# Performance work log

Hardware: AMD Instinct MI355X
Metric: run time of the kernel (lower is better)

Reference implementation:

```python
import jax, jax.numpy as jnp
import numpy as np

EPS = 1e-5

def _fm(x):
    # feature_map: exact (erf) GELU + 1, matching torch F.gelu default
    return jax.nn.gelu(x, approximate=False) + 1.0

def _gds(q, k):
    # global_dot_score: reduce over seq dim, broadcast back over seq
    e = (q * k).sum(axis=1)            # [B, D]
    return e[:, None, :] * q           # [B, S, D]

def _attn(q, k, v, scale):
    qf = _fm(q)
    kf = _fm(k)
    e = _gds(qf, kf) / scale           # [B, S, D]
    return jax.nn.softmax(e, axis=1) * v

def _ln(x, g, b):
    mu = x.mean(axis=-1, keepdims=True)
    var = ((x - mu) ** 2).mean(axis=-1, keepdims=True)
    return (x - mu) / jnp.sqrt(var + EPS) * g + b

def setup_inputs() -> dict:
    B, S, D, V, L, O = 8, 2048, 1024, 32000, 2, 2
    key = jax.random.key(0)
    ks = jax.random.split(key, 4)
    src = jax.random.randint(ks[0], (B, S), 0, V, dtype=jnp.int64 if jax.config.jax_enable_x64 else jnp.int32)
    trg = jax.random.randint(ks[1], (B, S), 0, V, dtype=src.dtype)
    emb = jax.random.normal(ks[2], (V, D), dtype=jnp.float32) * 0.02
    Wc = jax.random.normal(ks[3], (D, O), dtype=jnp.float32) * 0.02
    return {
        'src': src, 'trg': trg, 'emb': emb,
        'enc_g': jnp.ones((L, D), jnp.float32), 'enc_b': jnp.zeros((L, D), jnp.float32),
        'dec_ng': jnp.ones((L, D), jnp.float32), 'dec_nb': jnp.zeros((L, D), jnp.float32),
        'dec_tg': jnp.ones((L, D), jnp.float32), 'dec_tb': jnp.zeros((L, D), jnp.float32),
        'Wc': Wc, 'bc': jnp.zeros((O,), jnp.float32),
    }

def reference(src, trg, emb, enc_g, enc_b, dec_ng, dec_nb, dec_tg, dec_tb, Wc, bc):
    D = emb.shape[1]
    L = enc_g.shape[0]
    scale = jnp.sqrt(jnp.asarray(D, emb.dtype))

    # ---------- Encoder ----------
    x = emb[src]                          # [B, S, D]
    ctx = jnp.cumsum(x, axis=1)
    out = _gds(x, ctx)                    # encoder: out becomes rep
    rep = out
    for i in range(L):
        a = _attn(out, ctx, rep, scale)
        out = _ln(a + out, enc_g[i], enc_b[i])
        if i < L - 1:
            ctx = jnp.cumsum(out, axis=1)
            rep = _gds(out, ctx)
    enc_out = out
    enc_ctx = ctx[:, -1:, :]              # [B, 1, D]

    # ---------- Decoder ----------
    xe = emb[trg]
    ctx = jnp.cumsum(xe, axis=1)
    x = _gds(xe, ctx)                     # decoder: x becomes rep
    rep = x
    k2 = enc_ctx                          # [B, 1, D]
    v2 = enc_out.sum(axis=1, keepdims=True)  # [B, 1, D]
    for i in range(L):
        a1 = _attn(x, ctx, rep, scale)
        q = _ln(a1 + x, dec_ng[i], dec_nb[i])
        a2 = _attn(q, k2, v2, scale)      # cross attention (broadcast over seq)
        x = _ln(a2 + q, dec_tg[i], dec_tb[i])
        if i < L - 1:
            ctx = jnp.cumsum(x, axis=1)
            rep = _gds(x, ctx)

    # ---------- Predictor (use='seq', pool='mean') ----------
    pooled = x.mean(axis=1)               # [B, D]
    return pooled @ Wc + bc               # [B, out]
```

## Files before the change

kernel.cpp:

```cpp
#include <hip/hip_runtime.h>
#include <math.h>

namespace {

constexpr int Bb = 8;
constexpr int Ss = 2048;
constexpr int Dd = 1024;
constexpr int D4 = Dd / 4;
constexpr int NC = 256;
constexpr int Sc2 = Ss / NC;
constexpr int Tb = 256;
constexpr int SEG = 8;
constexpr int CPS = NC / SEG;
constexpr float INV_SCALE = 0.03125f;
constexpr float BIG = 3.0e38f;

__device__ __forceinline__ float fast_erf(float z) {
  float az = fabsf(z);
  float t = __builtin_amdgcn_rcpf(fmaf(0.3275911f, az, 1.0f));
  float p = fmaf(1.061405429f, t, -1.453152027f);
  p = fmaf(p, t, 1.421413741f);
  p = fmaf(p, t, -0.284496736f);
  p = fmaf(p, t, 0.254829592f);
  p *= t;
  float e = __expf(-az * az);
  float r = fmaf(-p, e, 1.0f);
  return copysignf(r, z);
}
__device__ __forceinline__ float fm_act(float x) {
  return fmaf(0.5f * x, 1.0f + fast_erf(x * 0.70710678118654752f), 1.0f);
}

__device__ __forceinline__ float4 f4(float v) { return make_float4(v, v, v, v); }
__device__ __forceinline__ float4 add4(float4 a, float4 b) {
  return make_float4(a.x + b.x, a.y + b.y, a.z + b.z, a.w + b.w);
}
__device__ __forceinline__ float4 mul4(float4 a, float4 b) {
  return make_float4(a.x * b.x, a.y * b.y, a.z * b.z, a.w * b.w);
}
__device__ __forceinline__ float4 fma4(float4 a, float4 b, float4 c) {
  return make_float4(fmaf(a.x, b.x, c.x), fmaf(a.y, b.y, c.y), fmaf(a.z, b.z, c.z), fmaf(a.w, b.w, c.w));
}
__device__ __forceinline__ float4 min4(float4 a, float4 b) {
  return make_float4(fminf(a.x, b.x), fminf(a.y, b.y), fminf(a.z, b.z), fminf(a.w, b.w));
}
__device__ __forceinline__ float4 max4(float4 a, float4 b) {
  return make_float4(fmaxf(a.x, b.x), fmaxf(a.y, b.y), fmaxf(a.z, b.z), fmaxf(a.w, b.w));
}
__device__ __forceinline__ float4 fm4(float4 x) {
  return make_float4(fm_act(x.x), fm_act(x.y), fm_act(x.z), fm_act(x.w));
}
__device__ __forceinline__ float4 ld4(const float* p, size_t j4) {
  return reinterpret_cast<const float4*>(p)[j4];
}
__device__ __forceinline__ void st4(float* p, size_t j4, float4 v) {
  reinterpret_cast<float4*>(p)[j4] = v;
}
__device__ __forceinline__ float4 pexp4(float4 ei, float4 qf, float4 M) {
  return make_float4(__expf(fmaf(ei.x, qf.x, -M.x)), __expf(fmaf(ei.y, qf.y, -M.y)),
                     __expf(fmaf(ei.z, qf.z, -M.z)), __expf(fmaf(ei.w, qf.w, -M.w)));
}

__device__ __forceinline__ float blockSum(float v) {
  __shared__ float wsm[Tb / 64];
  for (int off = 32; off > 0; off >>= 1) v += __shfl_down(v, off, 64);
  const int lane = threadIdx.x & 63;
  const int w = threadIdx.x >> 6;
  __syncthreads();
  if (lane == 0) wsm[w] = v;
  __syncthreads();
  return wsm[0] + wsm[1] + wsm[2] + wsm[3];
}

struct GA { const int* tok; float* X; float* cs; float* el; };
struct SA { const float* cs; const float* el; float* off; float* e; float* last; };
struct PA { const float* X; const float* qs; const float* off; float* pe; float* pmn; float* pmx; };
struct MA { const float* pe; const float* pmn; const float* pmx; const float* k2; float* ei; float* Mv; };
struct QA { const float* X; const float* qs; const float* ei; const float* Mv; float* ps; };
struct RA { const float* pp; float* outv; int recip; };
struct LA { float* X; const float* qs; const float* vs; const float* rs; const float* ml;
            const float* ei; const float* Mv; const float* rdv; const float* g; const float* bt;
            float* cs; float* el; float* xe; float* xn; float* xx; };


__global__ __launch_bounds__(Tb) void k_gather(GA a0, GA a1, const float* __restrict__ emb) {
  const GA a = (blockIdx.z == 0) ? a0 : a1;
  const int t = threadIdx.x, c = blockIdx.x, b = blockIdx.y;
  const int* tp = a.tok + b * Ss + c * Sc2;
  float4* xp = reinterpret_cast<float4*>(a.X) + ((size_t)(b * Ss + c * Sc2)) * D4 + t;
  const float4* ep = reinterpret_cast<const float4*>(emb);
  float4 run = f4(0.f), e = f4(0.f);
#pragma unroll
  for (int i = 0; i < Sc2; ++i) {
    float4 v = ep[(size_t)tp[i] * D4 + t];
    xp[(size_t)i * D4] = v;
    run = add4(run, v);
    e = fma4(v, run, e);
  }
  const size_t idx = ((size_t)b * NC + c) * D4 + t;
  st4(a.cs, idx, run);
  st4(a.el, idx, e);
}

__global__ __launch_bounds__(Tb) void k_p1(PA a0, PA a1) {
  const PA a = (blockIdx.z == 0) ? a0 : a1;
  const int t = threadIdx.x, c = blockIdx.x, b = blockIdx.y;
  const size_t idx = ((size_t)b * NC + c) * D4 + t;
  float4 run = ld4(a.off, idx);
  const float4 q4 = a.qs ? ld4(a.qs, (size_t)b * D4 + t) : f4(1.f);
  const float4* xp = reinterpret_cast<const float4*>(a.X) + ((size_t)(b * Ss + c * Sc2)) * D4 + t;
  float4 e = f4(0.f), mn = f4(BIG), mx = f4(0.f);
#pragma unroll
  for (int i = 0; i < Sc2; ++i) {
    float4 x = xp[(size_t)i * D4];
    run = add4(run, x);
    float4 qf = fm4(mul4(q4, x));
    float4 kf = fm4(run);
    e = fma4(qf, kf, e);
    mn = min4(mn, qf);
    mx = max4(mx, qf);
  }
  st4(a.pe, idx, e);
  st4(a.pmn, idx, mn);
  st4(a.pmx, idx, mx);
}

__global__ __launch_bounds__(Tb) void k_p2(QA a0, QA a1) {
  const QA a = (blockIdx.z == 0) ? a0 : a1;
  const int t = threadIdx.x, c = blockIdx.x, b = blockIdx.y;
  const size_t j4 = (size_t)b * D4 + t;
  const float4 q4 = a.qs ? ld4(a.qs, j4) : f4(1.f);
  const float4 e4 = ld4(a.ei, j4);
  const float4 M4 = ld4(a.Mv, j4);
  const float4* xp = reinterpret_cast<const float4*>(a.X) + ((size_t)(b * Ss + c * Sc2)) * D4 + t;
  float4 s = f4(0.f);
#pragma unroll
  for (int i = 0; i < Sc2; ++i) {
    float4 x = xp[(size_t)i * D4];
    float4 qf = fm4(mul4(q4, x));
    s = add4(s, pexp4(e4, qf, M4));
  }
  st4(a.ps, ((size_t)b * NC + c) * D4 + t, s);
}

__global__ __launch_bounds__(Tb) void k_ln(LA a0, LA a1) {
  const LA a = (blockIdx.z == 0) ? a0 : a1;
  __shared__ float red[Sc2][Tb];
  __shared__ float mu_s[Sc2], inv_s[Sc2];
  const int t = threadIdx.x, c = blockIdx.x, b = blockIdx.y;
  float4* xp = reinterpret_cast<float4*>(a.X) + ((size_t)(b * Ss + c * Sc2)) * D4 + t;
  const size_t j4 = (size_t)b * D4 + t;
  const float4 e4 = ld4(a.ei, j4), M4 = ld4(a.Mv, j4), rv4 = ld4(a.rdv, j4);
  const float4 q4 = a.qs ? ld4(a.qs, j4) : f4(1.f);
  const float4 vs4 = a.vs ? ld4(a.vs, j4) : f4(1.f);
  const float4 ml4 = a.ml ? ld4(a.ml, j4) : f4(1.f);
  const float4 rs4 = a.rs ? ld4(a.rs, j4) : f4(1.f);
  float4 vals[Sc2];
#pragma unroll
  for (int i = 0; i < Sc2; ++i) {
    float4 x = xp[(size_t)i * D4];
    float4 qf = fm4(mul4(q4, x));
    float4 p = mul4(pexp4(e4, qf, M4), rv4);
    float4 v = a.ml ? mul4(p, ml4) : mul4(p, mul4(vs4, x));
    float4 val = add4(v, mul4(rs4, x));
    vals[i] = val;
    red[i][t] = val.x + val.y + val.z + val.w;
  }
  __syncthreads();
  const int lane = t & 63, w = t >> 6;
#pragma unroll
  for (int rr = 0; rr < Sc2 / 4; ++rr) {
    const int row = w * (Sc2 / 4) + rr;
    float s = red[row][lane] + red[row][lane + 64] + red[row][lane + 128] + red[row][lane + 192];
    for (int off = 32; off > 0; off >>= 1) s += __shfl_down(s, off, 64);
    if (lane == 0) mu_s[row] = s * (1.0f / Dd);
  }
  __syncthreads();
#pragma unroll
  for (int i = 0; i < Sc2; ++i) {
    const float m = mu_s[i];
    float4 vv = vals[i];
    float aa = vv.x - m, b2 = vv.y - m, c2 = vv.z - m, d2 = vv.w - m;
    red[i][t] = aa * aa + b2 * b2 + c2 * c2 + d2 * d2;
  }
  __syncthreads();
#pragma unroll
  for (int rr = 0; rr < Sc2 / 4; ++rr) {
    const int row = w * (Sc2 / 4) + rr;
    float s = red[row][lane] + red[row][lane + 64] + red[row][lane + 128] + red[row][lane + 192];
    for (int off = 32; off > 0; off >>= 1) s += __shfl_down(s, off, 64);
    if (lane == 0) inv_s[row] = rsqrtf(s * (1.0f / Dd) + 1e-5f);
  }
  __syncthreads();
  const float4 g4 = ld4(a.g, t), b4 = ld4(a.bt, t);
  float4 run = f4(0.f), e = f4(0.f);
  float4 xs = f4(0.f), xmn = f4(BIG), xmx = f4(0.f);
#pragma unroll
  for (int i = 0; i < Sc2; ++i) {
    const float m = mu_s[i], inv = inv_s[i];
    float4 vv = vals[i];
    float4 y;
    y.x = fmaf((vv.x - m) * inv, g4.x, b4.x);
    y.y = fmaf((vv.y - m) * inv, g4.y, b4.y);
    y.z = fmaf((vv.z - m) * inv, g4.z, b4.z);
    y.w = fmaf((vv.w - m) * inv, g4.w, b4.w);
    xp[(size_t)i * D4] = y;
    if (a.cs) {
      run = add4(run, y);
      if (a.el) e = fma4(y, run, e);
    }
    if (a.xe) {
      float4 qfy = fm4(y);
      xs = add4(xs, qfy);
      xmn = min4(xmn, qfy);
      xmx = max4(xmx, qfy);
    }
  }
  const size_t idx = ((size_t)b * NC + c) * D4 + t;
  if (a.cs) st4(a.cs, idx, run);
  if (a.el) st4(a.el, idx, e);
  if (a.xe) {
    st4(a.xe, idx, xs);
    st4(a.xn, idx, xmn);
    st4(a.xx, idx, xmx);
  }
}


__global__ __launch_bounds__(Tb) void t_scan8(SA a0, SA a1) {
  const SA a = (blockIdx.z == 0) ? a0 : a1;
  __shared__ float lds[SEG][32];
  const int tid = threadIdx.x;
  const int jl = tid & 31, seg = tid >> 5;
  const int j = blockIdx.x * 32 + jl;
  const int b = j >> 10, d = j & 1023;
  const size_t base = (size_t)b * NC * Dd + d;
  float s = 0.f;
#pragma unroll 8
  for (int i = 0; i < CPS; ++i) s += a.cs[base + (size_t)(seg * CPS + i) * Dd];
  lds[seg][jl] = s;
  __syncthreads();
  float o = 0.f;
#pragma unroll
  for (int g2 = 0; g2 < SEG; ++g2) { float v = lds[g2][jl]; o += (g2 < seg) ? v : 0.f; }
  __syncthreads();
  float run = o, e = 0.f;
#pragma unroll 8
  for (int i = 0; i < CPS; ++i) {
    const size_t k = base + (size_t)(seg * CPS + i) * Dd;
    float cv = a.cs[k];
    a.off[k] = run;
    e += a.el[k] + run * cv;
    run += cv;
  }
  lds[seg][jl] = e;
  __syncthreads();
  if (seg == 0) {
    float et = 0.f;
#pragma unroll
    for (int g2 = 0; g2 < SEG; ++g2) et += lds[g2][jl];
    a.e[j] = et;
  }
  if (a.last && seg == SEG - 1) a.last[j] = run;
}

__global__ __launch_bounds__(Tb) void t_m8(MA a0, MA a1) {
  const MA a = (blockIdx.z == 0) ? a0 : a1;
  __shared__ float le[SEG][32], lmn[SEG][32], lmx[SEG][32];
  const int tid = threadIdx.x;
  const int jl = tid & 31, seg = tid >> 5;
  const int j = blockIdx.x * 32 + jl;
  const int b = j >> 10, d = j & 1023;
  const size_t base = (size_t)b * NC * Dd + d;
  float ec = 0.f, mn = BIG, mx = 0.f;
#pragma unroll 8
  for (int i = 0; i < CPS; ++i) {
    const size_t k = base + (size_t)(seg * CPS + i) * Dd;
    ec += a.pe[k];
    mn = fminf(mn, a.pmn[k]);
    mx = fmaxf(mx, a.pmx[k]);
  }
  le[seg][jl] = ec; lmn[seg][jl] = mn; lmx[seg][jl] = mx;
  __syncthreads();
  if (seg == 0) {
#pragma unroll
    for (int g2 = 1; g2 < SEG; ++g2) {
      ec += le[g2][jl];
      mn = fminf(mn, lmn[g2][jl]);
      mx = fmaxf(mx, lmx[g2][jl]);
    }
    if (a.k2) ec *= fm_act(a.k2[j]);
    const float e2 = ec * INV_SCALE;
    a.ei[j] = e2;
    a.Mv[j] = (ec >= 0.f) ? e2 * mx : e2 * mn;
  }
}

__global__ __launch_bounds__(Tb) void t_red8(RA a0, RA a1) {
  const RA a = (blockIdx.z == 0) ? a0 : a1;
  __shared__ float lds[SEG][32];
  const int tid = threadIdx.x;
  const int jl = tid & 31, seg = tid >> 5;
  const int j = blockIdx.x * 32 + jl;
  const int b = j >> 10, d = j & 1023;
  const size_t base = (size_t)b * NC * Dd + d;
  float s = 0.f;
#pragma unroll 8
  for (int i = 0; i < CPS; ++i) s += a.pp[base + (size_t)(seg * CPS + i) * Dd];
  lds[seg][jl] = s;
  __syncthreads();
  if (seg == 0) {
#pragma unroll
    for (int g2 = 1; g2 < SEG; ++g2) s += lds[g2][jl];
    a.outv[j] = a.recip ? 1.0f / s : s;
  }
}

__global__ __launch_bounds__(Tb) void k_final(const float* __restrict__ pooled, const float* __restrict__ Wc,
    const float* __restrict__ bc, float* __restrict__ out) {
  const int b = blockIdx.x, t = threadIdx.x;
  float4 acc = ld4(pooled, (size_t)b * D4 + t);
  float4 w0 = ld4(Wc, 2 * t), w1 = ld4(Wc, 2 * t + 1);
  float s0 = acc.x * w0.x + acc.y * w0.z + acc.z * w1.x + acc.w * w1.z;
  float s1 = acc.x * w0.y + acc.y * w0.w + acc.z * w1.y + acc.w * w1.w;
  s0 = blockSum(s0);
  s1 = blockSum(s1);
  if (t == 0) {
    out[b * 2 + 0] = s0 * (1.0f / Ss) + bc[0];
    out[b * 2 + 1] = s1 * (1.0f / Ss) + bc[1];
  }
}

}

extern "C" void kernel_launch(void* const* d_in, const int* in_sizes, int n_in,
                              void* d_out, int out_size, void* d_ws, size_t ws_size,
                              hipStream_t stream) {
  (void)in_sizes; (void)n_in; (void)out_size; (void)ws_size;
  const int* src = (const int*)d_in[0];
  const int* trg = (const int*)d_in[1];
  const float* emb = (const float*)d_in[2];
  const float* enc_g = (const float*)d_in[3];
  const float* enc_b = (const float*)d_in[4];
  const float* dec_ng = (const float*)d_in[5];
  const float* dec_nb = (const float*)d_in[6];
  const float* dec_tg = (const float*)d_in[7];
  const float* dec_tb = (const float*)d_in[8];
  const float* Wc = (const float*)d_in[9];
  const float* bc = (const float*)d_in[10];
  float* out = (float*)d_out;

  float* ws = (float*)d_ws;
  const size_t TEN = (size_t)Bb * Ss * Dd;
  const size_t MM = (size_t)Bb * NC * Dd;
  float* A0 = ws;
  float* A1 = A0 + TEN;
  float* p = A1 + TEN;
  float* csE = p; p += MM;  float* elE = p; p += MM;  float* offE = p; p += MM;
  float* peE = p; p += MM;  float* pmnE = p; p += MM; float* pmxE = p; p += MM;
  float* psE = p; p += MM;
  float* csD = p; p += MM;  float* elD = p; p += MM;  float* offD = p; p += MM;
  float* peD = p; p += MM;  float* pmnD = p; p += MM; float* pmxD = p; p += MM;
  float* psD = p; p += MM;
  const int BD = Bb * Dd;
  float* e0E = p; p += BD;  float* e1E = p; p += BD;
  float* e0D = p; p += BD;  float* e1D = p; p += BD;
  float* eiE = p; p += BD;  float* MvE = p; p += BD;  float* rdvE = p; p += BD;
  float* eiD = p; p += BD;  float* MvD = p; p += BD;  float* rdvD = p; p += BD;
  float* ectx = p; p += BD; float* v2 = p; p += BD;   float* pooled = p; p += BD;

  const dim3 g2(NC, Bb, 2), g1(NC, Bb, 1);
  const dim3 t2(BD / 32, 1, 2), t1(BD / 32, 1, 1);

  k_gather<<<g2, Tb, 0, stream>>>(GA{src, A0, csE, elE}, GA{trg, A1, csD, elD}, emb);
  t_scan8<<<t2, Tb, 0, stream>>>(SA{csE, elE, offE, e0E, nullptr}, SA{csD, elD, offD, e0D, nullptr});
  k_p1<<<g2, Tb, 0, stream>>>(PA{A0, e0E, offE, peE, pmnE, pmxE}, PA{A1, e0D, offD, peD, pmnD, pmxD});
  t_m8<<<t2, Tb, 0, stream>>>(MA{peE, pmnE, pmxE, nullptr, eiE, MvE}, MA{peD, pmnD, pmxD, nullptr, eiD, MvD});
  k_p2<<<g2, Tb, 0, stream>>>(QA{A0, e0E, eiE, MvE, psE}, QA{A1, e0D, eiD, MvD, psD});
  t_red8<<<t2, Tb, 0, stream>>>(RA{psE, rdvE, 1}, RA{psD, rdvD, 1});
  k_ln<<<g2, Tb, 0, stream>>>(
      LA{A0, e0E, e0E, e0E, nullptr, eiE, MvE, rdvE, enc_g, enc_b, csE, elE, nullptr, nullptr, nullptr},
      LA{A1, e0D, e0D, e0D, nullptr, eiD, MvD, rdvD, dec_ng, dec_nb, nullptr, nullptr, peD, pmnD, pmxD});

  t_scan8<<<t1, Tb, 0, stream>>>(SA{csE, elE, offE, e1E, ectx}, SA{csE, elE, offE, e1E, ectx});
  k_p1<<<g1, Tb, 0, stream>>>(PA{A0, nullptr, offE, peE, pmnE, pmxE}, PA{A0, nullptr, offE, peE, pmnE, pmxE});
  t_m8<<<t1, Tb, 0, stream>>>(MA{peE, pmnE, pmxE, nullptr, eiE, MvE}, MA{peE, pmnE, pmxE, nullptr, eiE, MvE});
  k_p2<<<g1, Tb, 0, stream>>>(QA{A0, nullptr, eiE, MvE, psE}, QA{A0, nullptr, eiE, MvE, psE});
  t_red8<<<t1, Tb, 0, stream>>>(RA{psE, rdvE, 1}, RA{psE, rdvE, 1});
  k_ln<<<g1, Tb, 0, stream>>>(
      LA{A0, nullptr, e1E, nullptr, nullptr, eiE, MvE, rdvE, enc_g + Dd, enc_b + Dd, csE, nullptr, nullptr, nullptr, nullptr},
      LA{A0, nullptr, e1E, nullptr, nullptr, eiE, MvE, rdvE, enc_g + Dd, enc_b + Dd, csE, nullptr, nullptr, nullptr, nullptr});
  t_red8<<<t1, Tb, 0, stream>>>(RA{csE, v2, 0}, RA{csE, v2, 0});

  t_m8<<<t1, Tb, 0, stream>>>(MA{peD, pmnD, pmxD, ectx, eiD, MvD}, MA{peD, pmnD, pmxD, ectx, eiD, MvD});
  k_p2<<<g1, Tb, 0, stream>>>(QA{A1, nullptr, eiD, MvD, psD}, QA{A1, nullptr, eiD, MvD, psD});
  t_red8<<<t1, Tb, 0, stream>>>(RA{psD, rdvD, 1}, RA{psD, rdvD, 1});
  k_ln<<<g1, Tb, 0, stream>>>(
      LA{A1, nullptr, nullptr, nullptr, v2, eiD, MvD, rdvD, dec_tg, dec_tb, csD, elD, nullptr, nullptr, nullptr},
      LA{A1, nullptr, nullptr, nullptr, v2, eiD, MvD, rdvD, dec_tg, dec_tb, csD, elD, nullptr, nullptr, nullptr});

  t_scan8<<<t1, Tb, 0, stream>>>(SA{csD, elD, offD, e1D, nullptr}, SA{csD, elD, offD, e1D, nullptr});
  k_p1<<<g1, Tb, 0, stream>>>(PA{A1, nullptr, offD, peD, pmnD, pmxD}, PA{A1, nullptr, offD, peD, pmnD, pmxD});
  t_m8<<<t1, Tb, 0, stream>>>(MA{peD, pmnD, pmxD, nullptr, eiD, MvD}, MA{peD, pmnD, pmxD, nullptr, eiD, MvD});
  k_p2<<<g1, Tb, 0, stream>>>(QA{A1, nullptr, eiD, MvD, psD}, QA{A1, nullptr, eiD, MvD, psD});
  t_red8<<<t1, Tb, 0, stream>>>(RA{psD, rdvD, 1}, RA{psD, rdvD, 1});
  k_ln<<<g1, Tb, 0, stream>>>(
      LA{A1, nullptr, e1D, nullptr, nullptr, eiD, MvD, rdvD, dec_ng + Dd, dec_nb + Dd, nullptr, nullptr, peD, pmnD, pmxD},
      LA{A1, nullptr, e1D, nullptr, nullptr, eiD, MvD, rdvD, dec_ng + Dd, dec_nb + Dd, nullptr, nullptr, peD, pmnD, pmxD});

  t_m8<<<t1, Tb, 0, stream>>>(MA{peD, pmnD, pmxD, ectx, eiD, MvD}, MA{peD, pmnD, pmxD, ectx, eiD, MvD});
  k_p2<<<g1, Tb, 0, stream>>>(QA{A1, nullptr, eiD, MvD, psD}, QA{A1, nullptr, eiD, MvD, psD});
  t_red8<<<t1, Tb, 0, stream>>>(RA{psD, rdvD, 1}, RA{psD, rdvD, 1});
  k_ln<<<g1, Tb, 0, stream>>>(
      LA{A1, nullptr, nullptr, nullptr, v2, eiD, MvD, rdvD, dec_tg + Dd, dec_tb + Dd, csD, nullptr, nullptr, nullptr, nullptr},
      LA{A1, nullptr, nullptr, nullptr, v2, eiD, MvD, rdvD, dec_tg + Dd, dec_tb + Dd, csD, nullptr, nullptr, nullptr, nullptr});

  t_red8<<<t1, Tb, 0, stream>>>(RA{csD, pooled, 0}, RA{csD, pooled, 0});
  k_final<<<Bb, Tb, 0, stream>>>(pooled, Wc, bc, out);
}
```

Baseline: 476.4 us.

## Merge encoder layer-2 and decoder cross-attn stats launches, skip unused final LN stores

Adds a flag to the layernorm kernel so the last encoder layer and last decoder layer skip writing the normalized activations, since only their column sums are consumed afterward. The decoder's first cross-attention statistics kernels (m8, p2, red8) are hoisted and batched with the encoder's second-layer statistics into combined two-slice launches. This is possible because they depend only on ectx and the decoder's first LN output. Together these cut about 32MB of global writes per skipped store and three kernel launches, while filling more of the GPU per launch.

```diff
diff --git a/kernel.cpp b/kernel.cpp
--- a/kernel.cpp
+++ b/kernel.cpp
@@ -80,7 +80,7 @@
 struct RA { const float* pp; float* outv; int recip; };
 struct LA { float* X; const float* qs; const float* vs; const float* rs; const float* ml;
             const float* ei; const float* Mv; const float* rdv; const float* g; const float* bt;
-            float* cs; float* el; float* xe; float* xn; float* xx; };
+            float* cs; float* el; float* xe; float* xn; float* xx; int wout; };
 
 
 __global__ __launch_bounds__(Tb) void k_gather(GA a0, GA a1, const float* __restrict__ emb) {
@@ -204,7 +204,7 @@
     y.y = fmaf((vv.y - m) * inv, g4.y, b4.y);
     y.z = fmaf((vv.z - m) * inv, g4.z, b4.z);
     y.w = fmaf((vv.w - m) * inv, g4.w, b4.w);
-    xp[(size_t)i * D4] = y;
+    if (a.wout) xp[(size_t)i * D4] = y;
     if (a.cs) {
       run = add4(run, y);
       if (a.el) e = fma4(y, run, e);
@@ -379,25 +379,23 @@
   k_p2<<<g2, Tb, 0, stream>>>(QA{A0, e0E, eiE, MvE, psE}, QA{A1, e0D, eiD, MvD, psD});
   t_red8<<<t2, Tb, 0, stream>>>(RA{psE, rdvE, 1}, RA{psD, rdvD, 1});
   k_ln<<<g2, Tb, 0, stream>>>(
-      LA{A0, e0E, e0E, e0E, nullptr, eiE, MvE, rdvE, enc_g, enc_b, csE, elE, nullptr, nullptr, nullptr},
-      LA{A1, e0D, e0D, e0D, nullptr, eiD, MvD, rdvD, dec_ng, dec_nb, nullptr, nullptr, peD, pmnD, pmxD});
+      LA{A0, e0E, e0E, e0E, nullptr, eiE, MvE, rdvE, enc_g, enc_b, csE, elE, nullptr, nullptr, nullptr, 1},
+      LA{A1, e0D, e0D, e0D, nullptr, eiD, MvD, rdvD, dec_ng, dec_nb, nullptr, nullptr, peD, pmnD, pmxD, 1});
 
   t_scan8<<<t1, Tb, 0, stream>>>(SA{csE, elE, offE, e1E, ectx}, SA{csE, elE, offE, e1E, ectx});
   k_p1<<<g1, Tb, 0, stream>>>(PA{A0, nullptr, offE, peE, pmnE, pmxE}, PA{A0, nullptr, offE, peE, pmnE, pmxE});
-  t_m8<<<t1, Tb, 0, stream>>>(MA{peE, pmnE, pmxE, nullptr, eiE, MvE}, MA{peE, pmnE, pmxE, nullptr, eiE, MvE});
-  k_p2<<<g1, Tb, 0, stream>>>(QA{A0, nullptr, eiE, MvE, psE}, QA{A0, nullptr, eiE, MvE, psE});
-  t_red8<<<t1, Tb, 0, stream>>>(RA{psE, rdvE, 1}, RA{psE, rdvE, 1});
+
+  t_m8<<<t2, Tb, 0, stream>>>(MA{peE, pmnE, pmxE, nullptr, eiE, MvE}, MA{peD, pmnD, pmxD, ectx, eiD, MvD});
+  k_p2<<<g2, Tb, 0, stream>>>(QA{A0, nullptr, eiE, MvE, psE}, QA{A1, nullptr, eiD, MvD, psD});
+  t_red8<<<t2, Tb, 0, stream>>>(RA{psE, rdvE, 1}, RA{psD, rdvD, 1});
   k_ln<<<g1, Tb, 0, stream>>>(
-      LA{A0, nullptr, e1E, nullptr, nullptr, eiE, MvE, rdvE, enc_g + Dd, enc_b + Dd, csE, nullptr, nullptr, nullptr, nullptr},
-      LA{A0, nullptr, e1E, nullptr, nullptr, eiE, MvE, rdvE, enc_g + Dd, enc_b + Dd, csE, nullptr, nullptr, nullptr, nullptr});
+      LA{A0, nullptr, e1E, nullptr, nullptr, eiE, MvE, rdvE, enc_g + Dd, enc_b + Dd, csE, nullptr, nullptr, nullptr, nullptr, 0},
+      LA{A0, nullptr, e1E, nullptr, nullptr, eiE, MvE, rdvE, enc_g + Dd, enc_b + Dd, csE, nullptr, nullptr, nullptr, nullptr, 0});
   t_red8<<<t1, Tb, 0, stream>>>(RA{csE, v2, 0}, RA{csE, v2, 0});
 
-  t_m8<<<t1, Tb, 0, stream>>>(MA{peD, pmnD, pmxD, ectx, eiD, MvD}, MA{peD, pmnD, pmxD, ectx, eiD, MvD});
-  k_p2<<<g1, Tb, 0, stream>>>(QA{A1, nullptr, eiD, MvD, psD}, QA{A1, nullptr, eiD, MvD, psD});
-  t_red8<<<t1, Tb, 0, stream>>>(RA{psD, rdvD, 1}, RA{psD, rdvD, 1});
   k_ln<<<g1, Tb, 0, stream>>>(
-      LA{A1, nullptr, nullptr, nullptr, v2, eiD, MvD, rdvD, dec_tg, dec_tb, csD, elD, nullptr, nullptr, nullptr},
-      LA{A1, nullptr, nullptr, nullptr, v2, eiD, MvD, rdvD, dec_tg, dec_tb, csD, elD, nullptr, nullptr, nullptr});
+      LA{A1, nullptr, nullptr, nullptr, v2, eiD, MvD, rdvD, dec_tg, dec_tb, csD, elD, nullptr, nullptr, nullptr, 1},
+      LA{A1, nullptr, nullptr, nullptr, v2, eiD, MvD, rdvD, dec_tg, dec_tb, csD, elD, nullptr, nullptr, nullptr, 1});
 
   t_scan8<<<t1, Tb, 0, stream>>>(SA{csD, elD, offD, e1D, nullptr}, SA{csD, elD, offD, e1D, nullptr});
   k_p1<<<g1, Tb, 0, stream>>>(PA{A1, nullptr, offD, peD, pmnD, pmxD}, PA{A1, nullptr, offD, peD, pmnD, pmxD});
@@ -405,15 +403,15 @@
   k_p2<<<g1, Tb, 0, stream>>>(QA{A1, nullptr, eiD, MvD, psD}, QA{A1, nullptr, eiD, MvD, psD});
   t_red8<<<t1, Tb, 0, stream>>>(RA{psD, rdvD, 1}, RA{psD, rdvD, 1});
   k_ln<<<g1, Tb, 0, stream>>>(
-      LA{A1, nullptr, e1D, nullptr, nullptr, eiD, MvD, rdvD, dec_ng + Dd, dec_nb + Dd, nullptr, nullptr, peD, pmnD, pmxD},
-      LA{A1, nullptr, e1D, nullptr, nullptr, eiD, MvD, rdvD, dec_ng + Dd, dec_nb + Dd, nullptr, nullptr, peD, pmnD, pmxD});
+      LA{A1, nullptr, e1D, nullptr, nullptr, eiD, MvD, rdvD, dec_ng + Dd, dec_nb + Dd, nullptr, nullptr, peD, pmnD, pmxD, 1},
+      LA{A1, nullptr, e1D, nullptr, nullptr, eiD, MvD, rdvD, dec_ng + Dd, dec_nb + Dd, nullptr, nullptr, peD, pmnD, pmxD, 1});
 
   t_m8<<<t1, Tb, 0, stream>>>(MA{peD, pmnD, pmxD, ectx, eiD, MvD}, MA{peD, pmnD, pmxD, ectx, eiD, MvD});
   k_p2<<<g1, Tb, 0, stream>>>(QA{A1, nullptr, eiD, MvD, psD}, QA{A1, nullptr, eiD, MvD, psD});
   t_red8<<<t1, Tb, 0, stream>>>(RA{psD, rdvD, 1}, RA{psD, rdvD, 1});
   k_ln<<<g1, Tb, 0, stream>>>(
-      LA{A1, nullptr, nullptr, nullptr, v2, eiD, MvD, rdvD, dec_tg + Dd, dec_tb + Dd, csD, nullptr, nullptr, nullptr, nullptr},
-      LA{A1, nullptr, nullptr, nullptr, v2, eiD, MvD, rdvD, dec_tg + Dd, dec_tb + Dd, csD, nullptr, nullptr, nullptr, nullptr});
+      LA{A1, nullptr, nullptr, nullptr, v2, eiD, MvD, rdvD, dec_tg + Dd, dec_tb + Dd, csD, nullptr, nullptr, nullptr, nullptr, 0},
+      LA{A1, nullptr, nullptr, nullptr, v2, eiD, MvD, rdvD, dec_tg + Dd, dec_tb + Dd, csD, nullptr, nullptr, nullptr, nullptr, 0});
 
   t_red8<<<t1, Tb, 0, stream>>>(RA{csD, pooled, 0}, RA{csD, pooled, 0});
   k_final<<<Bb, Tb, 0, stream>>>(pooled, Wc, bc, out);
```

Measured after the change: 454.2 us. -4.7%, faster.
